# Optimization experiments

Measured on AMD Instinct MI355X. Metric: run time of the kernel, lower is better.

Reference implementation:

```python
import jax, jax.numpy as jnp
import numpy as np

N_TOK, D_MODEL, N_EXPERTS, TOP_K = 8192, 512, 8, 2


def setup_inputs() -> dict:
    key = jax.random.key(0)
    k1, k2, k3 = jax.random.split(key, 3)
    x = jax.random.normal(k1, (N_TOK, D_MODEL), jnp.float32)
    w_gate = jax.random.normal(k2, (D_MODEL, N_EXPERTS), jnp.float32) * 0.02
    expert_w = jax.random.normal(k3, (N_EXPERTS, D_MODEL, D_MODEL), jnp.float32) * (D_MODEL ** -0.5)
    return {"x": x, "w_gate": w_gate, "expert_w": expert_w, "top_k": TOP_K}


def _cv_sq(v):
    m = jnp.mean(v)
    return jnp.var(v) / (m * m + 1e-10)


def reference(x, w_gate, expert_w, top_k):
    # ---- Gate (clean top-k gating, eval mode of noisy-top-k) ----
    logits = x @ w_gate                              # [N, E]
    top_vals, top_idx = jax.lax.top_k(logits, top_k)  # [N, k]
    top_gates = jax.nn.softmax(top_vals, axis=-1)
    n, e = logits.shape
    gates = jnp.zeros((n, e), x.dtype).at[jnp.arange(n)[:, None], top_idx].set(top_gates)

    # ---- dispatch -> per-expert GEMM -> log-domain combine ----
    # combine(): stitched = cat(expert_out).exp() * nonzero_gates; index_add over
    # batch index; zeros -> eps; log. Dense-equivalent (tokens with gate 0
    # contribute exactly nothing):
    expert_out = jnp.einsum('nd,edf->nef', x, expert_w)   # per-expert outputs [N, E, D]
    combined = jnp.einsum('ne,nef->nf', gates, jnp.exp(expert_out))  # [N, D]
    eps = np.float32(np.finfo(np.float64).eps)
    combined = jnp.where(combined == 0, eps, combined)
    out = jnp.log(combined)

    # ---- load-balance aux loss: cv^2(importance) + cv^2(load) ----
    importance = gates.sum(0)
    load = (gates > 0).sum(0).astype(x.dtype)
    balance_loss = _cv_sq(importance) + _cv_sq(load)
    return out, balance_loss
```

## Files before the change

kernel.cpp:

```cpp
#include <hip/hip_runtime.h>
#include <hip/hip_bf16.h>
#include <math.h>

#define N_TOK 8192
#define D 512
#define NE 8

typedef float f32x4 __attribute__((ext_vector_type(4)));
typedef __bf16 bf16x8 __attribute__((ext_vector_type(8)));
typedef unsigned short u16;
typedef u16 u16x8 __attribute__((ext_vector_type(8)));

#define OFF_TOKE  256
#define OFF_TOKG  65792
#define OFF_BUCK  131328
#define OFF_XB    (1u << 20)
#define OFF_EWT   (OFF_XB + 8u * 1024 * 1024)
#define OFF_Y     (OFF_EWT + 4u * 1024 * 1024)

__device__ __forceinline__ u16 f2b(float v) {
    __hip_bfloat16 h = __float2bfloat16(v);
    return *reinterpret_cast<u16*>(&h);
}
__device__ __forceinline__ float b2f(u16 u) {
    __hip_bfloat16 h;
    *reinterpret_cast<u16*>(&h) = u;
    return __bfloat162float(h);
}

typedef __attribute__((address_space(1))) const void* gp1_t;
typedef __attribute__((address_space(3))) void* lp3_t;
__device__ __forceinline__ void gload16(const void* g, void* l) {
    __builtin_amdgcn_global_load_lds((gp1_t)g, (lp3_t)l, 16, 0, 0);
}

__global__ __launch_bounds__(256) void gate_prep_kernel(
    const float* __restrict__ x, const float* __restrict__ wg,
    const float* __restrict__ ew,
    int* __restrict__ tok_e, float* __restrict__ tok_g, u16* __restrict__ xb,
    u16* __restrict__ ewt)
{
    __shared__ __align__(16) float sbuf[64 * 65];
    int b = blockIdx.x;
    int tid = threadIdx.x;

    if (b >= 2048) {
        int pb = b - 2048;
        float (*tile)[65] = (float(*)[65])sbuf;
        int e = pb >> 6, dt = (pb >> 3) & 7, ftl = pb & 7;
        int c = tid & 63, rq = tid >> 6;
        const float* src = ew + (size_t)e * D * D + (size_t)(dt * 64) * D + ftl * 64;
#pragma unroll
        for (int i = 0; i < 16; ++i) {
            int r = i * 4 + rq;
            tile[r][c] = src[(size_t)r * D + c];
        }
        __syncthreads();
        u16* dst = ewt + (size_t)e * D * D + (size_t)(ftl * 64) * D + dt * 64;
#pragma unroll
        for (int i = 0; i < 16; ++i) {
            int f = i * 4 + rq;
            dst[(size_t)f * D + c] = f2b(tile[c][f]);
        }
        return;
    }

    float* wgs = sbuf;
    for (int i = tid; i < NE * D; i += 256) {
        int d = i >> 3, e = i & 7;
        wgs[e * D + d] = wg[i];
    }
    __syncthreads();

    int wave = tid >> 6, lane = tid & 63;
    int n = b * 4 + wave;
    const float* xr = x + (size_t)n * D;
    u16* xbr = xb + (size_t)n * D;

    float p[NE];
#pragma unroll
    for (int e = 0; e < NE; ++e) p[e] = 0.f;
#pragma unroll
    for (int it = 0; it < 8; ++it) {
        float xv = xr[it * 64 + lane];
        xbr[it * 64 + lane] = f2b(xv);
#pragma unroll
        for (int e = 0; e < NE; ++e)
            p[e] += xv * wgs[e * D + it * 64 + lane];
    }
#pragma unroll
    for (int off = 32; off > 0; off >>= 1) {
#pragma unroll
        for (int e = 0; e < NE; ++e)
            p[e] += __shfl_xor(p[e], off);
    }

    if (lane == 0) {
        int e1 = 0; float v1 = p[0];
#pragma unroll
        for (int e = 1; e < NE; ++e) if (p[e] > v1) { v1 = p[e]; e1 = e; }
        int e2 = -1; float v2 = -INFINITY;
#pragma unroll
        for (int e = 0; e < NE; ++e) if (e != e1 && p[e] > v2) { v2 = p[e]; e2 = e; }
        float t = __expf(v2 - v1);
        float inv = 1.f / (1.f + t);
        tok_e[2 * n] = e1;     tok_e[2 * n + 1] = e2;
        tok_g[2 * n] = inv;    tok_g[2 * n + 1] = t * inv;
    }
}

__global__ __launch_bounds__(256) void bucketize_kernel(
    const int* __restrict__ tok_e, const float* __restrict__ tok_g,
    int* __restrict__ count, float* __restrict__ imp, int* __restrict__ bucket)
{
    __shared__ int lcnt[NE], lbase[NE];
    __shared__ float limp[NE];
    int tid = threadIdx.x;
    if (tid < NE) { lcnt[tid] = 0; limp[tid] = 0.f; }
    __syncthreads();

    int n = blockIdx.x * 256 + tid;
    int e1 = tok_e[2 * n], e2 = tok_e[2 * n + 1];
    float g1 = tok_g[2 * n], g2 = tok_g[2 * n + 1];
    int o1 = atomicAdd(&lcnt[e1], 1);
    int o2 = atomicAdd(&lcnt[e2], 1);
    atomicAdd(&limp[e1], g1);
    atomicAdd(&limp[e2], g2);
    __syncthreads();
    if (tid < NE) {
        lbase[tid] = atomicAdd(&count[tid], lcnt[tid]);
        atomicAdd(&imp[tid], limp[tid]);
    }
    __syncthreads();
    bucket[e1 * N_TOK + lbase[e1] + o1] = 2 * n;
    bucket[e2 * N_TOK + lbase[e2] + o2] = 2 * n + 1;
}

__global__ __launch_bounds__(256) void moe_gemm(
    const u16* __restrict__ xb, const u16* __restrict__ ewt,
    const int* __restrict__ count, const int* __restrict__ bucket,
    u16* __restrict__ y)
{
    int b = blockIdx.x;
    int ft = b & 3;
    int tt = (b >> 2) & 127;
    int e  = b >> 9;
    int cnt = count[e];
    if (tt * 64 >= cnt) return;

    __shared__ int sl[64];
    __shared__ __align__(16) u16 smem[9216];

    int tid = threadIdx.x;
    if (tid < 64) {
        int idx = tt * 64 + tid;
        sl[tid] = (idx < cnt) ? bucket[e * N_TOK + idx] : -1;
    }
    __syncthreads();

    int w = tid >> 6, l = tid & 63;
    int c8 = (l & 3) * 8;
    int ra = w * 16 + (l >> 2);
    int sa = sl[ra];
    const u16* gA = xb + (size_t)((sa < 0) ? 0 : (sa >> 1)) * D + c8;
    u16* lA = &smem[w * 512];
    int fb0 = w * 32 + (l >> 2);
    const u16* gB0 = ewt + ((size_t)e * D + ft * 128 + fb0) * D + c8;
    const u16* gB1 = gB0 + (size_t)16 * D;
    u16* lB0 = &smem[2048 + w * 1024];
    u16* lB1 = lB0 + 512;

    int wm = w & 1, wn = w >> 1;
    int lm = l & 15, quad = l >> 4, kq = quad * 8;

    f32x4 acc[2][4] = {};

    for (int kc = 0; kc < 16; ++kc) {
        __syncthreads();
        gload16(gA + kc * 32, lA);
        gload16(gB0 + kc * 32, lB0);
        gload16(gB1 + kc * 32, lB1);
        __syncthreads();

        bf16x8 af[2], bfv[4];
#pragma unroll
        for (int i = 0; i < 2; ++i)
            af[i] = *(const bf16x8*)&smem[(wm * 32 + i * 16 + lm) * 32 + kq];
#pragma unroll
        for (int j = 0; j < 4; ++j)
            bfv[j] = *(const bf16x8*)&smem[2048 + (wn * 64 + j * 16 + lm) * 32 + kq];
#pragma unroll
        for (int i = 0; i < 2; ++i)
#pragma unroll
            for (int j = 0; j < 4; ++j)
                acc[i][j] = __builtin_amdgcn_mfma_f32_16x16x32_bf16(
                    af[i], bfv[j], acc[i][j], 0, 0, 0);
    }

    __syncthreads();
    u16* Es = smem + w * 2304;
#pragma unroll
    for (int i = 0; i < 2; ++i)
#pragma unroll
        for (int j = 0; j < 4; ++j)
#pragma unroll
            for (int r = 0; r < 4; ++r)
                Es[(i * 16 + quad * 4 + r) * 72 + j * 16 + lm] =
                    f2b(acc[i][j][r]);
    int row = l >> 1, hc = l & 1;
    int s = sl[wm * 32 + row];
    const u16* src = Es + row * 72 + hc * 32;
    u16* dst = y + (size_t)((s < 0) ? 0 : s) * D + ft * 128 + wn * 64 + hc * 32;
    if (s >= 0) {
#pragma unroll
        for (int c = 0; c < 4; ++c)
            *(u16x8*)(dst + c * 8) = *(const u16x8*)(src + c * 8);
    }
}

__global__ __launch_bounds__(256) void combine_kernel(
    const u16* __restrict__ y, const float* __restrict__ tok_g,
    const int* __restrict__ count, const float* __restrict__ imp,
    float* __restrict__ out)
{
    if (blockIdx.x == 2048) {
        if (threadIdx.x == 0) {
            float mi = 0.f, ml = 0.f;
            for (int e = 0; e < NE; ++e) { mi += imp[e]; ml += (float)count[e]; }
            mi *= 0.125f; ml *= 0.125f;
            float vi = 0.f, vl = 0.f;
            for (int e = 0; e < NE; ++e) {
                float di = imp[e] - mi;          vi += di * di;
                float dl = (float)count[e] - ml; vl += dl * dl;
            }
            vi *= 0.125f; vl *= 0.125f;
            out[N_TOK * D] = vi / (mi * mi + 1e-10f) + vl / (ml * ml + 1e-10f);
        }
        return;
    }
    int idx = blockIdx.x * 256 + threadIdx.x;
    int n = idx >> 6;
    int c = (idx & 63) * 8;
    const u16x8 ua = *(const u16x8*)(y + (size_t)(2 * n) * D + c);
    const u16x8 ub = *(const u16x8*)(y + (size_t)(2 * n + 1) * D + c);
    float g1 = tok_g[2 * n], g2 = tok_g[2 * n + 1];
    const float eps = 2.2204460492503131e-16f;
    float r[8];
#pragma unroll
    for (int i = 0; i < 8; ++i) {
        float v = g1 * __expf(b2f(ua[i])) + g2 * __expf(b2f(ub[i]));
        r[i] = __logf(v == 0.f ? eps : v);
    }
    float* o = out + (size_t)n * D + c;
    *(float4*)(o)     = *(float4*)&r[0];
    *(float4*)(o + 4) = *(float4*)&r[4];
}

extern "C" void kernel_launch(void* const* d_in, const int* in_sizes, int n_in,
                              void* d_out, int out_size, void* d_ws, size_t ws_size,
                              hipStream_t stream)
{
    const float* x  = (const float*)d_in[0];
    const float* wg = (const float*)d_in[1];
    const float* ew = (const float*)d_in[2];
    char* ws = (char*)d_ws;
    int*   count  = (int*)(ws + 0);
    float* imp    = (float*)(ws + 64);
    int*   tok_e  = (int*)(ws + OFF_TOKE);
    float* tok_g  = (float*)(ws + OFF_TOKG);
    int*   bucket = (int*)(ws + OFF_BUCK);
    u16*   xb     = (u16*)(ws + OFF_XB);
    u16*   ewt    = (u16*)(ws + OFF_EWT);
    u16*   y      = (u16*)(ws + OFF_Y);
    float* out    = (float*)d_out;

    hipMemsetAsync(ws, 0, 128, stream);
    gate_prep_kernel<<<2048 + 512, 256, 0, stream>>>(x, wg, ew, tok_e, tok_g, xb, ewt);
    bucketize_kernel<<<N_TOK / 256, 256, 0, stream>>>(tok_e, tok_g, count, imp, bucket);
    moe_gemm<<<NE * 128 * 4, 256, 0, stream>>>(xb, ewt, count, bucket, y);
    combine_kernel<<<2049, 256, 0, stream>>>(y, tok_g, count, imp, out);
}
```

Before: 127.9 us.

## Keep gathered A tile resident in LDS and loop over output column tiles

```diff
diff --git a/kernel.cpp b/kernel.cpp
--- a/kernel.cpp
+++ b/kernel.cpp
@@ -142,14 +142,15 @@
     u16* __restrict__ y)
 {
     int b = blockIdx.x;
-    int ft = b & 3;
-    int tt = (b >> 2) & 127;
-    int e  = b >> 9;
+    int e  = b >> 7;
+    int tt = b & 127;
     int cnt = count[e];
     if (tt * 64 >= cnt) return;
 
+    __shared__ __align__(16) u16 Asm[32768];
+    __shared__ __align__(16) u16 Bsm[16384];
+    __shared__ __align__(16) u16 Es[9216];
     __shared__ int sl[64];
-    __shared__ __align__(16) u16 smem[9216];
 
     int tid = threadIdx.x;
     if (tid < 64) {
@@ -160,61 +161,77 @@
 
     int w = tid >> 6, l = tid & 63;
     int c8 = (l & 3) * 8;
-    int ra = w * 16 + (l >> 2);
-    int sa = sl[ra];
+
+    int ar = w * 16 + (l >> 2);
+    int sa = sl[ar];
     const u16* gA = xb + (size_t)((sa < 0) ? 0 : (sa >> 1)) * D + c8;
-    u16* lA = &smem[w * 512];
+    u16* lA = &Asm[w * 512 + l * 8];
+#pragma unroll
+    for (int p = 0; p < 16; ++p)
+        gload16(gA + p * 32, lA + p * 2048);
+
     int fb0 = w * 32 + (l >> 2);
-    const u16* gB0 = ewt + ((size_t)e * D + ft * 128 + fb0) * D + c8;
-    const u16* gB1 = gB0 + (size_t)16 * D;
-    u16* lB0 = &smem[2048 + w * 1024];
+    u16* lB0 = &Bsm[w * 1024 + l * 8];
     u16* lB1 = lB0 + 512;
 
     int wm = w & 1, wn = w >> 1;
     int lm = l & 15, quad = l >> 4, kq = quad * 8;
 
-    f32x4 acc[2][4] = {};
-
-    for (int kc = 0; kc < 16; ++kc) {
-        __syncthreads();
-        gload16(gA + kc * 32, lA);
-        gload16(gB0 + kc * 32, lB0);
-        gload16(gB1 + kc * 32, lB1);
-        __syncthreads();
-
-        bf16x8 af[2], bfv[4];
+    for (int ft = 0; ft < 4; ++ft) {
+        const u16* gB0 = ewt + ((size_t)e * D + ft * 128 + fb0) * D + c8;
+        const u16* gB1 = gB0 + (size_t)16 * D;
+
+        f32x4 acc[2][4] = {};
+
+        for (int kc = 0; kc < 4; ++kc) {
+            __syncthreads();
+#pragma unroll
+            for (int q = 0; q < 4; ++q) {
+                int ko = kc * 128 + q * 32;
+                gload16(gB0 + ko, lB0 + q * 4096);
+                gload16(gB1 + ko, lB1 + q * 4096);
+            }
+            __syncthreads();
+
+#pragma unroll
+            for (int ks = 0; ks < 4; ++ks) {
+                int pl = kc * 4 + ks;
+                bf16x8 af[2], bfv[4];
+#pragma unroll
+                for (int i = 0; i < 2; ++i)
+                    af[i] = *(const bf16x8*)
+                        &Asm[pl * 2048 + (wm * 32 + i * 16 + lm) * 32 + kq];
+#pragma unroll
+                for (int j = 0; j < 4; ++j)
+                    bfv[j] = *(const bf16x8*)
+                        &Bsm[ks * 4096 + (wn * 64 + j * 16 + lm) * 32 + kq];
+#pragma unroll
+                for (int i = 0; i < 2; ++i)
+#pragma unroll
+                    for (int j = 0; j < 4; ++j)
+                        acc[i][j] = __builtin_amdgcn_mfma_f32_16x16x32_bf16(
+                            af[i], bfv[j], acc[i][j], 0, 0, 0);
+            }
+        }
+
+        u16* Ew = Es + w * 2304;
 #pragma unroll
         for (int i = 0; i < 2; ++i)
-            af[i] = *(const bf16x8*)&smem[(wm * 32 + i * 16 + lm) * 32 + kq];
-#pragma unroll
-        for (int j = 0; j < 4; ++j)
-            bfv[j] = *(const bf16x8*)&smem[2048 + (wn * 64 + j * 16 + lm) * 32 + kq];
-#pragma unroll
-        for (int i = 0; i < 2; ++i)
 #pragma unroll
             for (int j = 0; j < 4; ++j)
-                acc[i][j] = __builtin_amdgcn_mfma_f32_16x16x32_bf16(
-                    af[i], bfv[j], acc[i][j], 0, 0, 0);
-    }
-
-    __syncthreads();
-    u16* Es = smem + w * 2304;
-#pragma unroll
-    for (int i = 0; i < 2; ++i)
-#pragma unroll
-        for (int j = 0; j < 4; ++j)
-#pragma unroll
-            for (int r = 0; r < 4; ++r)
-                Es[(i * 16 + quad * 4 + r) * 72 + j * 16 + lm] =
-                    f2b(acc[i][j][r]);
-    int row = l >> 1, hc = l & 1;
-    int s = sl[wm * 32 + row];
-    const u16* src = Es + row * 72 + hc * 32;
-    u16* dst = y + (size_t)((s < 0) ? 0 : s) * D + ft * 128 + wn * 64 + hc * 32;
-    if (s >= 0) {
-#pragma unroll
-        for (int c = 0; c < 4; ++c)
-            *(u16x8*)(dst + c * 8) = *(const u16x8*)(src + c * 8);
+#pragma unroll
+                for (int r = 0; r < 4; ++r)
+                    Ew[(i * 16 + quad * 4 + r) * 72 + j * 16 + lm] =
+                        f2b(acc[i][j][r]);
+        int row = l >> 1, hc = l & 1;
+        int s = sl[wm * 32 + row];
+        const u16* src = Ew + row * 72 + hc * 32;
+        if (s >= 0) {
+            u16* dst = y + (size_t)s * D + ft * 128 + wn * 64 + hc * 32;
+#pragma unroll
+            for (int c = 0; c < 4; ++c)
+                *(u16x8*)(dst + c * 8) = *(const u16x8*)(src + c * 8);
+        }
     }
 }
 
@@ -277,6 +294,6 @@
     hipMemsetAsync(ws, 0, 128, stream);
     gate_prep_kernel<<<2048 + 512, 256, 0, stream>>>(x, wg, ew, tok_e, tok_g, xb, ewt);
     bucketize_kernel<<<N_TOK / 256, 256, 0, stream>>>(tok_e, tok_g, count, imp, bucket);
-    moe_gemm<<<NE * 128 * 4, 256, 0, stream>>>(xb, ewt, count, bucket, y);
+    moe_gemm<<<NE * 128, 256, 0, stream>>>(xb, ewt, count, bucket, y);
     combine_kernel<<<2049, 256, 0, stream>>>(y, tok_g, count, imp, out);
 }
```

Measured after the change: 140.9 us. 10.2% more time.
